# Kernel tuning notes

Hardware: AMD Instinct MI355X
Metric: run time of the kernel (lower is better)

The kernel has to match this reference:

```python
import jax, jax.numpy as jnp
import numpy as np

N, E, C, H, EDGE_DIM, HID = 50000, 800000, 128, 8, 64, 512
D = C // H  # head dim = out_channels_conv


def layer_norm(x, g, b, eps=1e-5):
    mu = x.mean(-1, keepdims=True)
    var = ((x - mu) ** 2).mean(-1, keepdims=True)
    return (x - mu) * jax.lax.rsqrt(var + eps) * g + b


def _lin_init(k, fan_in, fan_out):
    s = 1.0 / np.sqrt(fan_in)
    kw, kb = jax.random.split(k)
    w = jax.random.uniform(kw, (fan_in, fan_out), minval=-s, maxval=s, dtype=jnp.float32)
    b = jax.random.uniform(kb, (fan_out,), minval=-s, maxval=s, dtype=jnp.float32)
    return w, b


def setup_inputs() -> dict:
    key = jax.random.key(0)
    ks = jax.random.split(key, 16)
    wq, bq = _lin_init(ks[0], C, C)
    wk, bk = _lin_init(ks[1], C, C)
    wv, bv = _lin_init(ks[2], C, C)
    ws, bs = _lin_init(ks[3], C, C)          # lin_self
    we, be = _lin_init(ks[4], EDGE_DIM, C)   # lin_edge
    wp, bp = _lin_init(ks[5], C, C)          # projection
    w1, b1 = _lin_init(ks[6], C, HID)        # node_dst_mlp[0]
    w2, b2 = _lin_init(ks[7], HID, C)        # node_dst_mlp[2]
    x = jax.random.normal(ks[8], (N, C), dtype=jnp.float32)
    edge_attr = jax.random.normal(ks[9], (E, EDGE_DIM), dtype=jnp.float32)
    edge_index = jax.random.randint(ks[10], (2, E), 0, N, dtype=jnp.int64)
    return dict(
        x=x, edge_attr=edge_attr, edge_index=edge_index,
        wq=wq, bq=bq, wk=wk, bk=bk, wv=wv, bv=bv, ws=ws, bs=bs,
        we=we, be=be, wp=wp, bp=bp, w1=w1, b1=b1, w2=w2, b2=b2,
        ln1_g=jnp.ones((C,), jnp.float32), ln1_b=jnp.zeros((C,), jnp.float32),
        ln2_g=jnp.ones((C,), jnp.float32), ln2_b=jnp.zeros((C,), jnp.float32),
    )


def reference(x, edge_attr, edge_index,
              wq, bq, wk, bk, wv, bv, ws, bs, we, be, wp, bp,
              w1, b1, w2, b2, ln1_g, ln1_b, ln2_g, ln2_b):
    src, dst = edge_index[0], edge_index[1]

    x_skip = x
    xn = layer_norm(x, ln1_g, ln1_b)                       # layer_norm_attention
    x_r = xn @ ws + bs                                     # lin_self residual
    q = (xn @ wq + bq).reshape(N, H, D)
    k = (xn @ wk + bk).reshape(N, H, D)
    v = (xn @ wv + bv).reshape(N, H, D)
    e = (edge_attr @ we + be).reshape(E, H, D)             # lin_edge (edge_pre_mlp = Identity)

    # edge-indexed multi-head attention: softmax over incoming edges per dst node
    ke = k[src] + e                                        # [E,H,D]
    alpha = jnp.einsum('ehd,ehd->eh', q[dst], ke) / np.sqrt(D)   # [E,H]
    amax = jax.lax.stop_gradient(jax.ops.segment_max(alpha, dst, num_segments=N))
    ex = jnp.exp(alpha - amax[dst])
    den = jax.ops.segment_sum(ex, dst, num_segments=N)
    w = ex / (den[dst] + 1e-16)                            # [E,H]
    out = jax.ops.segment_sum(w[:, :, None] * (v[src] + e), dst, num_segments=N)  # [N,H,D]
    out = out.reshape(N, C)

    out = (out + x_r) @ wp + bp                            # projection
    out = out + x_skip
    h = layer_norm(out, ln2_g, ln2_b)                      # layer_norm_mlp_dst
    h = jax.nn.gelu(h @ w1 + b1) @ w2 + b2                 # node_dst_mlp
    nodes_new = out + h
    return nodes_new, edge_attr
```

## Files before the change

### kernel.cpp

```cpp
#include <hip/hip_runtime.h>
#include <hip/hip_bf16.h>
#include <cstdio>

#define NN 50000
#define NE 800000
#define CC 128
#define EDIM 64
#define HIDN 512

using bf16 = __hip_bfloat16;
typedef short sh8 __attribute__((ext_vector_type(8)));
typedef float f32x4 __attribute__((ext_vector_type(4)));

static __device__ __forceinline__ float b2f(bf16 v){ return __bfloat162float(v); }
static __device__ __forceinline__ bf16 f2b(float v){ return __float2bfloat16(v); }
static __device__ __forceinline__ float u2f(unsigned short u){
    union { unsigned int i; float f; } w; w.i = ((unsigned int)u) << 16; return w.f;
}
static __device__ __forceinline__ unsigned short f2u(float f){
    bf16 b = __float2bfloat16(f);
    return *reinterpret_cast<unsigned short*>(&b);
}
static __device__ __forceinline__ float2 loadbf2(const bf16* p){
    __hip_bfloat162 v = *reinterpret_cast<const __hip_bfloat162*>(p);
    return make_float2(__bfloat162float(v.x), __bfloat162float(v.y));
}
static __device__ __forceinline__ float gelu_tanh(float x){
    const float c = 0.7978845608028654f;
    float u = c * (x + 0.044715f * x * x * x);
    return x / (1.0f + __expf(-2.0f * u));
}

constexpr size_t AL(size_t x){ return (x + 255) & ~(size_t)255; }
constexpr size_t OFF_FLAG = 0;
constexpr size_t OFF_DEG  = 256;
constexpr size_t OFF_ROW  = AL(OFF_DEG + (size_t)(NN + 1) * 4);
constexpr size_t OFF_CUR  = AL(OFF_ROW + (size_t)(NN + 1) * 4);
constexpr size_t OFF_SRC  = AL(OFF_CUR + (size_t)(NN + 1) * 4);
constexpr size_t OFF_DST  = AL(OFF_SRC + (size_t)NE * 4);
constexpr size_t OFF_QC   = AL(OFF_DST + (size_t)NE * 4);
constexpr size_t OFF_KC   = AL(OFF_QC  + (size_t)NN * CC * 2);
constexpr size_t OFF_VC   = AL(OFF_KC  + (size_t)NN * CC * 2);
constexpr size_t OFF_ATT  = AL(OFF_VC  + (size_t)NN * CC * 2);
constexpr size_t OFF_PRM  = AL(OFF_ATT + (size_t)NN * CC * 2);
constexpr size_t PRM_ELEMS = 4096;
constexpr size_t OFF_ALP  = AL(OFF_PRM + PRM_ELEMS * 2);
constexpr size_t OFF_VP   = AL(OFF_ALP + (size_t)NE * 8 * 2);
constexpr size_t OFF_XRC  = AL(OFF_VP + (size_t)NE * CC * 2);
constexpr size_t OFF_WFQ  = AL(OFF_XRC + (size_t)NN * CC * 2);
constexpr size_t OFF_WFK  = OFF_WFQ + 32768;
constexpr size_t OFF_WFV  = OFF_WFK + 32768;
constexpr size_t OFF_WFS  = OFF_WFV + 32768;
constexpr size_t OFF_WFP  = OFF_WFS + 32768;
constexpr size_t OFF_WF1  = OFF_WFP + 32768;
constexpr size_t OFF_WF2  = OFF_WF1 + 131072;
constexpr size_t OFF_WFE  = OFF_WF2 + 131072;
constexpr size_t OFF_BSUM = OFF_WFE + 16384;
constexpr size_t WS_NEED  = OFF_BSUM + 256;

__global__ void k_detect(const unsigned short* xw, const unsigned int* ew, int* flags){
    __shared__ int sw, sz;
    if (threadIdx.x == 0){ sw = 0; sz = 0; }
    __syncthreads();
    int w = 0;
    for (int i = threadIdx.x; i < 8192; i += 256){
        unsigned e = (xw[i] >> 7) & 0xFF;
        if (e == 0xFF || (e != 0 && (e < 0x60 || e > 0x90))) w++;
    }
    atomicAdd(&sw, w);
    int z = 0;
    for (int i = threadIdx.x; i < 2048; i += 256)
        if (ew[2*i+1] == 0u) z++;
    atomicAdd(&sz, z);
    __syncthreads();
    if (threadIdx.x == 0){
        flags[0] = (sw > 2048) ? 1 : 0;
        flags[1] = (sz > 1536) ? 1 : 0;
    }
}

struct CvtJob { const void* s; bf16* d; int n; };
struct CvtJobs { CvtJob j[12]; };
__global__ void k_cvt_all(CvtJobs jobs, const int* flags){
    const int f = flags[0];
    const int e = blockIdx.x >> 1;
    const CvtJob J = jobs.j[e];
    const int stride = 2 * 256;
    for (int i = (blockIdx.x & 1) * 256 + threadIdx.x; i < J.n; i += stride){
        if (f) J.d[i] = f2b(((const float*)J.s)[i]);
        else   J.d[i] = ((const bf16*)J.s)[i];
    }
}

__global__ void k_cvt_idx(const int* e32, int* srcI, int* dstI, int* deg, const int* flags){
    const int f = flags[1];
    int i = blockIdx.x * blockDim.x + threadIdx.x;
    const int stride = gridDim.x * blockDim.x;
    if (f){
        const long long* e64 = (const long long*)e32;
        for (; i < NE; i += stride){
            srcI[i] = (int)e64[i];
            const int d = (int)e64[NE + i];
            dstI[i] = d;
            atomicAdd(&deg[d], 1);
        }
    } else {
        for (; i < NE; i += stride){
            srcI[i] = e32[i];
            const int d = e32[NE + i];
            dstI[i] = d;
            atomicAdd(&deg[d], 1);
        }
    }
}

struct WJob { const void* W; bf16* WF; int K; int N; };
struct WJobs { WJob j[8]; };
__global__ void k_wprep_all(WJobs jobs, const int* flags){
    const int f = flags[0];
    const WJob J = jobs.j[blockIdx.x / 48];
    const int KS = J.K >> 5;
    const int total = J.K * J.N;
    for (int o = (blockIdx.x % 48) * 256 + threadIdx.x; o < total; o += 48 * 256){
        const int j  = o & 7;
        const int ln = (o >> 3) & 63;
        const int tt = o >> 9;
        const int ks = tt % KS, ct = tt / KS;
        const int kk = (ks << 5) + ((ln >> 4) << 3) + j;
        const int c  = (ct << 4) + (ln & 15);
        const int src = kk * J.N + c;
        J.WF[o] = f ? f2b(((const float*)J.W)[src]) : ((const bf16*)J.W)[src];
    }
}

#define ASWZ(row, chunk)  (((row) << 8)  + ((((chunk) ^ ((row) & 15))) << 4))
#define HSWZ(row, chunk)  (((row) << 10) + ((((chunk) ^ ((row) & 15))) << 4))
#define EASWZ(row, chunk) (((row) << 7)  + ((((chunk) ^ ((row) & 7)))  << 4))

static __device__ __forceinline__ void gemm_nodes_128(
    const unsigned short* Abase, int row0, int lane,
    const bf16* __restrict__ WF, const bf16* __restrict__ bias,
    bf16* __restrict__ outp, int n0)
{
    const int rA = row0 + (lane & 15);
    sh8 af[4];
    #pragma unroll
    for (int ks = 0; ks < 4; ++ks)
        af[ks] = *(const sh8*)((const char*)Abase + ASWZ(rA, (ks << 2) + (lane >> 4)));
    f32x4 acc[8] = {};
    #pragma unroll
    for (int ks = 0; ks < 4; ++ks)
        #pragma unroll
        for (int ct = 0; ct < 8; ++ct){
            sh8 bfr = *(const sh8*)(WF + ((size_t)((ct << 2) + ks) * 64 + lane) * 8);
            acc[ct] = __builtin_amdgcn_mfma_f32_16x16x32_bf16(af[ks], bfr, acc[ct], 0, 0, 0);
        }
    #pragma unroll
    for (int ct = 0; ct < 8; ++ct){
        const int c = (ct << 4) + (lane & 15);
        const float bv = b2f(bias[c]);
        #pragma unroll
        for (int i = 0; i < 4; ++i){
            const int r = row0 + ((lane >> 4) << 2) + i;
            if (n0 + r < NN)
                outp[(size_t)(n0 + r) * CC + c] = f2b(acc[ct][i] + bv);
        }
    }
}

__global__ __launch_bounds__(256) void k_node_pre2(
    const void* __restrict__ x_raw, const int* __restrict__ flags,
    const bf16* __restrict__ WFq, const bf16* __restrict__ bq,
    const bf16* __restrict__ WFk, const bf16* __restrict__ bk,
    const bf16* __restrict__ WFv, const bf16* __restrict__ bv,
    const bf16* __restrict__ WFs, const bf16* __restrict__ bs,
    const bf16* __restrict__ g,  const bf16* __restrict__ bb,
    bf16* __restrict__ q, bf16* __restrict__ k, bf16* __restrict__ v,
    bf16* __restrict__ xr)
{
    __shared__ unsigned short A[64 * 128];
    const int t = threadIdx.x, lane = t & 63, wid = t >> 6;
    const int n0 = blockIdx.x * 64;
    const int row0 = wid * 16;

    if (flags[0]){
        const float* x = (const float*)x_raw;
        #pragma unroll
        for (int it = 0; it < 8; ++it){
            const int idx = lane + 64 * it;
            const int row = row0 + (idx >> 5), c = (idx & 31) << 2;
            float4 a = make_float4(0.f, 0.f, 0.f, 0.f);
            if (n0 + row < NN)
                a = *(const float4*)&x[(size_t)(n0 + row) * CC + c];
            ushort4 b;
            b.x = f2u(a.x); b.y = f2u(a.y); b.z = f2u(a.z); b.w = f2u(a.w);
            *(ushort4*)((char*)A + ASWZ(row, c >> 3) + ((c & 7) << 1)) = b;
        }
    } else {
        const bf16* x = (const bf16*)x_raw;
        #pragma unroll
        for (int it = 0; it < 4; ++it){
            const int idx = lane + 64 * it;
            const int row = row0 + (idx >> 4), chunk = idx & 15, col = chunk << 3;
            uint4 val = make_uint4(0u, 0u, 0u, 0u);
            if (n0 + row < NN)
                val = *(const uint4*)&x[(size_t)(n0 + row) * CC + col];
            *(uint4*)((char*)A + ASWZ(row, chunk)) = val;
        }
    }

    {
        const int nd = row0 + (lane & 15), qd = lane >> 4;
        float vals[32];
        #pragma unroll
        for (int i = 0; i < 4; ++i){
            uint4 u = *(const uint4*)((const char*)A + ASWZ(nd, (qd << 2) + i));
            unsigned uu[4] = {u.x, u.y, u.z, u.w};
            #pragma unroll
            for (int j2 = 0; j2 < 4; ++j2){
                vals[i*8 + j2*2]     = u2f((unsigned short)(uu[j2] & 0xFFFF));
                vals[i*8 + j2*2 + 1] = u2f((unsigned short)(uu[j2] >> 16));
            }
        }
        float s = 0.f;
        #pragma unroll
        for (int i = 0; i < 32; ++i) s += vals[i];
        s += __shfl_xor(s, 16); s += __shfl_xor(s, 32);
        const float mu = s * (1.0f / CC);
        float vv = 0.f;
        #pragma unroll
        for (int i = 0; i < 32; ++i){ const float d = vals[i] - mu; vv += d * d; }
        vv += __shfl_xor(vv, 16); vv += __shfl_xor(vv, 32);
        const float rstd = rsqrtf(vv * (1.0f / CC) + 1e-5f);
        #pragma unroll
        for (int i = 0; i < 4; ++i){
            unsigned w[4];
            #pragma unroll
            for (int j2 = 0; j2 < 4; ++j2){
                const int c0 = qd * 32 + i * 8 + j2 * 2;
                const float a0 = (vals[i*8+j2*2]   - mu) * rstd * b2f(g[c0])   + b2f(bb[c0]);
                const float a1 = (vals[i*8+j2*2+1] - mu) * rstd * b2f(g[c0+1]) + b2f(bb[c0+1]);
                w[j2] = (unsigned)f2u(a0) | ((unsigned)f2u(a1) << 16);
            }
            *(uint4*)((char*)A + ASWZ(nd, (qd << 2) + i)) = make_uint4(w[0], w[1], w[2], w[3]);
        }
    }

    gemm_nodes_128(A, row0, lane, WFq, bq, q,  n0);
    gemm_nodes_128(A, row0, lane, WFk, bk, k,  n0);
    gemm_nodes_128(A, row0, lane, WFv, bv, v,  n0);
    gemm_nodes_128(A, row0, lane, WFs, bs, xr, n0);
}

__global__ __launch_bounds__(1024) void k_scan1(const int* __restrict__ deg,
                                                int* __restrict__ row, int* __restrict__ bsum){
    __shared__ int sb[1024];
    const int t = threadIdx.x;
    const int idx = blockIdx.x * 1024 + t;
    sb[t] = (idx < NN) ? deg[idx] : 0;
    __syncthreads();
    for (int off = 1; off < 1024; off <<= 1){
        int tv = (t >= off) ? sb[t - off] : 0;
        __syncthreads();
        sb[t] += tv;
        __syncthreads();
    }
    if (idx < NN) row[idx + 1] = sb[t];
    if (t == 1023) bsum[blockIdx.x] = sb[1023];
}

__global__ __launch_bounds__(1024) void k_scan3(const int* __restrict__ bsum,
                                                int* __restrict__ row, int* __restrict__ cur){
    __shared__ int sadd;
    const int t = threadIdx.x;
    if (t < 64){
        int a = 0;
        for (int i = t; i < (int)blockIdx.x; i += 64) a += bsum[i];
        for (int off = 32; off; off >>= 1) a += __shfl_xor(a, off);
        if (t == 0) sadd = a;
    }
    __syncthreads();
    const int idx = blockIdx.x * 1024 + t;
    if (idx < NN){
        const int vfin = row[idx + 1] + sadd;
        row[idx + 1] = vfin;
        cur[idx + 1] = vfin;
    }
    if (idx == 0){ row[0] = 0; cur[0] = 0; }
}

__global__ __launch_bounds__(256) void k_edge4(
    const void* __restrict__ ea_raw, const int* __restrict__ flags,
    const bf16* __restrict__ WFe, const bf16* __restrict__ be,
    const bf16* __restrict__ kv_q, const bf16* __restrict__ kv_k, const bf16* __restrict__ kv_v,
    const int* __restrict__ srcI, const int* __restrict__ dstI, int* __restrict__ cur,
    unsigned short* __restrict__ alphap, unsigned short* __restrict__ vperm,
    void* __restrict__ outv)
{
    __shared__ unsigned short EA[64 * 64];
    __shared__ unsigned short ET[64 * 128];
    const int t = threadIdx.x, lane = t & 63, wid = t >> 6;
    const int e0 = blockIdx.x * 64;
    const int row0 = wid * 16;

    if (flags[0]){
        const float* ea = (const float*)ea_raw;
        float* outd = (float*)outv + (size_t)NN * CC;
        #pragma unroll
        for (int it = 0; it < 4; ++it){
            const int idx = lane + 64 * it;
            const int row = row0 + (idx >> 4), c = (idx & 15) << 2;
            const size_t o = (size_t)(e0 + row) * EDIM + c;
            const float4 a = *(const float4*)&ea[o];
            *(float4*)&outd[o] = a;
            ushort4 b;
            b.x = f2u(a.x); b.y = f2u(a.y); b.z = f2u(a.z); b.w = f2u(a.w);
            *(ushort4*)((char*)EA + EASWZ(row, c >> 3) + ((c & 7) << 1)) = b;
        }
    } else {
        const unsigned short* ea = (const unsigned short*)ea_raw;
        unsigned short* outd = (unsigned short*)outv + (size_t)NN * CC;
        #pragma unroll
        for (int it = 0; it < 2; ++it){
            const int idx = lane + 64 * it;
            const int row = row0 + (idx >> 3), c = (idx & 7) << 3;
            const size_t o = (size_t)(e0 + row) * EDIM + c;
            uint4 raw = *(const uint4*)&ea[o];
            *(uint4*)&outd[o] = raw;
            *(uint4*)((char*)EA + EASWZ(row, c >> 3)) = raw;
        }
    }

    {
        const int rA = row0 + (lane & 15);
        sh8 af[2];
        #pragma unroll
        for (int ks = 0; ks < 2; ++ks)
            af[ks] = *(const sh8*)((const char*)EA + EASWZ(rA, (ks << 2) + (lane >> 4)));
        f32x4 acc[8] = {};
        #pragma unroll
        for (int ks = 0; ks < 2; ++ks)
            #pragma unroll
            for (int ct = 0; ct < 8; ++ct){
                sh8 bfr = *(const sh8*)(WFe + ((size_t)((ct << 1) + ks) * 64 + lane) * 8);
                acc[ct] = __builtin_amdgcn_mfma_f32_16x16x32_bf16(af[ks], bfr, acc[ct], 0, 0, 0);
            }
        #pragma unroll
        for (int ct = 0; ct < 8; ++ct){
            const int c = (ct << 4) + (lane & 15);
            const float bv = b2f(be[c]);
            #pragma unroll
            for (int i = 0; i < 4; ++i){
                const int r = row0 + ((lane >> 4) << 2) + i;
                *(unsigned short*)((char*)ET + ASWZ(r, c >> 3) + ((c & 7) << 1)) =
                    f2u(acc[ct][i] + bv);
            }
        }
    }

    const int g = t >> 5, cT = t & 31, c = cT << 2;
    int s8[8], d8[8];
    #pragma unroll
    for (int i = 0; i < 8; ++i){
        const int eid = e0 + g * 8 + i;
        s8[i] = srcI[eid];
        d8[i] = dstI[eid];
    }
    int pmine = 0;
    if (cT < 8) pmine = atomicAdd(&cur[dstI[e0 + g * 8 + cT]], 1);
    int p8[8];
    #pragma unroll
    for (int i = 0; i < 8; ++i)
        p8[i] = __shfl(pmine, ((g & 1) << 5) + i);

    ushort4 kr[8], vr[8], qr[8];
    #pragma unroll
    for (int i = 0; i < 8; ++i) kr[i] = *(const ushort4*)&kv_k[(size_t)s8[i] * CC + c];
    #pragma unroll
    for (int i = 0; i < 8; ++i) vr[i] = *(const ushort4*)&kv_v[(size_t)s8[i] * CC + c];
    #pragma unroll
    for (int i = 0; i < 8; ++i) qr[i] = *(const ushort4*)&kv_q[(size_t)d8[i] * CC + c];
    #pragma unroll
    for (int i = 0; i < 8; ++i){
        const ushort4 ev = *(const ushort4*)((const char*)ET + ASWZ(g * 8 + i, c >> 3) + ((c & 7) << 1));
        const float e0_ = u2f(ev.x), e1_ = u2f(ev.y), e2_ = u2f(ev.z), e3_ = u2f(ev.w);
        float part = u2f(qr[i].x) * (e0_ + u2f(kr[i].x)) + u2f(qr[i].y) * (e1_ + u2f(kr[i].y))
                   + u2f(qr[i].z) * (e2_ + u2f(kr[i].z)) + u2f(qr[i].w) * (e3_ + u2f(kr[i].w));
        part += __shfl_xor(part, 1);
        part += __shfl_xor(part, 2);
        if ((cT & 3) == 0)
            alphap[(size_t)p8[i] * 8 + (cT >> 2)] = f2u(part * 0.25f);
        ushort4 vo;
        vo.x = f2u(e0_ + u2f(vr[i].x)); vo.y = f2u(e1_ + u2f(vr[i].y));
        vo.z = f2u(e2_ + u2f(vr[i].z)); vo.w = f2u(e3_ + u2f(vr[i].w));
        *(ushort4*)&vperm[(size_t)p8[i] * CC + c] = vo;
    }
}

__global__ __launch_bounds__(256) void k_attn3(
    const unsigned short* __restrict__ alphap, const bf16* __restrict__ vperm,
    const int* __restrict__ rowstart, bf16* __restrict__ attn_bf)
{
    const int t = threadIdx.x, lane = t & 63, wid = t >> 6;
    const int n = blockIdx.x * 4 + wid;
    const int h = lane >> 3;

    float m = -INFINITY, den = 0.0f;
    float2 num = make_float2(0.0f, 0.0f);

    const int jb = rowstart[n], je = rowstart[n + 1];
    for (int j = jb; j < je; ++j) {
        const float alpha = u2f(alphap[(size_t)j * 8 + h]);
        const float2 v2 = loadbf2(&vperm[(size_t)j * CC + 2 * lane]);
        if (alpha > m) {
            const float sc = __expf(m - alpha);
            den *= sc; num.x *= sc; num.y *= sc;
            m = alpha;
        }
        const float p = __expf(alpha - m);
        den += p;
        num.x += p * v2.x;
        num.y += p * v2.y;
    }
    const float inv = 1.0f / (den + 1e-16f);
    __hip_bfloat162 pr;
    pr.x = f2b(num.x * inv);
    pr.y = f2b(num.y * inv);
    *reinterpret_cast<__hip_bfloat162*>(&attn_bf[(size_t)n * CC + 2 * lane]) = pr;
}

__global__ __launch_bounds__(256) void k_post2(
    const bf16* __restrict__ attn_bf, const bf16* __restrict__ xr,
    const void* __restrict__ x_raw,
    const bf16* __restrict__ WFp, const bf16* __restrict__ bp,
    const bf16* __restrict__ WF1, const bf16* __restrict__ b1,
    const bf16* __restrict__ WF2, const bf16* __restrict__ b2c,
    const bf16* __restrict__ g2, const bf16* __restrict__ bb2,
    void* __restrict__ outv, const int* __restrict__ flags)
{
    __shared__ unsigned short A[64 * 128];
    __shared__ unsigned short HID[64 * 512];
    const int t = threadIdx.x, lane = t & 63, wid = t >> 6;
    const int n0 = blockIdx.x * 64;
    const int f32io = flags[0];
    const int row0 = wid * 16;

    #pragma unroll
    for (int it = 0; it < 4; ++it){
        const int idx = lane + 64 * it;
        const int row = row0 + (idx >> 4), chunk = idx & 15, col = chunk << 3;
        unsigned w[4] = {0u, 0u, 0u, 0u};
        if (n0 + row < NN){
            const size_t o = (size_t)(n0 + row) * CC + col;
            uint4 a4 = *(const uint4*)&attn_bf[o];
            uint4 r4 = *(const uint4*)&xr[o];
            unsigned au[4] = {a4.x, a4.y, a4.z, a4.w};
            unsigned ru[4] = {r4.x, r4.y, r4.z, r4.w};
            #pragma unroll
            for (int j2 = 0; j2 < 4; ++j2){
                const float lo = u2f((unsigned short)(au[j2] & 0xFFFF)) +
                                 u2f((unsigned short)(ru[j2] & 0xFFFF));
                const float hi = u2f((unsigned short)(au[j2] >> 16)) +
                                 u2f((unsigned short)(ru[j2] >> 16));
                w[j2] = (unsigned)f2u(lo) | ((unsigned)f2u(hi) << 16);
            }
        }
        *(uint4*)((char*)A + ASWZ(row, chunk)) = make_uint4(w[0], w[1], w[2], w[3]);
    }

    const int rA = row0 + (lane & 15);

    float out2[8][4];
    {
        sh8 af[4];
        #pragma unroll
        for (int ks = 0; ks < 4; ++ks)
            af[ks] = *(const sh8*)((const char*)A + ASWZ(rA, (ks << 2) + (lane >> 4)));
        f32x4 acc[8] = {};
        #pragma unroll
        for (int ks = 0; ks < 4; ++ks)
            #pragma unroll
            for (int ct = 0; ct < 8; ++ct){
                sh8 bfr = *(const sh8*)(WFp + ((size_t)((ct << 2) + ks) * 64 + lane) * 8);
                acc[ct] = __builtin_amdgcn_mfma_f32_16x16x32_bf16(af[ks], bfr, acc[ct], 0, 0, 0);
            }
        #pragma unroll
        for (int ct = 0; ct < 8; ++ct){
            const int c = (ct << 4) + (lane & 15);
            const float bv = b2f(bp[c]);
            #pragma unroll
            for (int i = 0; i < 4; ++i){
                const int r = row0 + ((lane >> 4) << 2) + i;
                float xs = 0.f;
                if (n0 + r < NN){
                    const size_t o = (size_t)(n0 + r) * CC + c;
                    xs = f32io ? ((const float*)x_raw)[o] : b2f(((const bf16*)x_raw)[o]);
                }
                out2[ct][i] = acc[ct][i] + bv + xs;
            }
        }
    }

    {
        float mu[4], rstd[4];
        #pragma unroll
        for (int i = 0; i < 4; ++i){
            float s = 0.f;
            #pragma unroll
            for (int ct = 0; ct < 8; ++ct) s += out2[ct][i];
            s += __shfl_xor(s, 1); s += __shfl_xor(s, 2);
            s += __shfl_xor(s, 4); s += __shfl_xor(s, 8);
            mu[i] = s * (1.0f / CC);
        }
        #pragma unroll
        for (int i = 0; i < 4; ++i){
            float vv = 0.f;
            #pragma unroll
            for (int ct = 0; ct < 8; ++ct){ const float d = out2[ct][i] - mu[i]; vv += d * d; }
            vv += __shfl_xor(vv, 1); vv += __shfl_xor(vv, 2);
            vv += __shfl_xor(vv, 4); vv += __shfl_xor(vv, 8);
            rstd[i] = rsqrtf(vv * (1.0f / CC) + 1e-5f);
        }
        #pragma unroll
        for (int ct = 0; ct < 8; ++ct){
            const int c = (ct << 4) + (lane & 15);
            const float gv = b2f(g2[c]), bbv = b2f(bb2[c]);
            const int chunk = c >> 3;
            #pragma unroll
            for (int i = 0; i < 4; ++i){
                const int r = row0 + ((lane >> 4) << 2) + i;
                const float ln = (out2[ct][i] - mu[i]) * rstd[i] * gv + bbv;
                *(unsigned short*)((char*)A + ASWZ(r, chunk) + ((c & 7) << 1)) = f2u(ln);
            }
        }
    }

    {
        sh8 af[4];
        #pragma unroll
        for (int ks = 0; ks < 4; ++ks)
            af[ks] = *(const sh8*)((const char*)A + ASWZ(rA, (ks << 2) + (lane >> 4)));
        #pragma unroll
        for (int grp = 0; grp < 4; ++grp){
            f32x4 acc[8] = {};
            #pragma unroll
            for (int ks = 0; ks < 4; ++ks)
                #pragma unroll
                for (int ctl = 0; ctl < 8; ++ctl){
                    const int ct = grp * 8 + ctl;
                    sh8 bfr = *(const sh8*)(WF1 + ((size_t)((ct << 2) + ks) * 64 + lane) * 8);
                    acc[ctl] = __builtin_amdgcn_mfma_f32_16x16x32_bf16(af[ks], bfr, acc[ctl], 0, 0, 0);
                }
            #pragma unroll
            for (int ctl = 0; ctl < 8; ++ctl){
                const int ct = grp * 8 + ctl;
                const int c = (ct << 4) + (lane & 15);
                const float bv = b2f(b1[c]);
                const int chunk = c >> 3;
                #pragma unroll
                for (int i = 0; i < 4; ++i){
                    const int r = row0 + ((lane >> 4) << 2) + i;
                    const float h = gelu_tanh(acc[ctl][i] + bv);
                    *(unsigned short*)((char*)HID + HSWZ(r, chunk) + ((c & 7) << 1)) = f2u(h);
                }
            }
        }
    }

    {
        f32x4 acc[8] = {};
        #pragma unroll
        for (int ks = 0; ks < 16; ++ks){
            sh8 afh = *(const sh8*)((const char*)HID + HSWZ(rA, (ks << 2) + (lane >> 4)));
            #pragma unroll
            for (int ct = 0; ct < 8; ++ct){
                sh8 bfr = *(const sh8*)(WF2 + ((size_t)((ct << 4) + ks) * 64 + lane) * 8);
                acc[ct] = __builtin_amdgcn_mfma_f32_16x16x32_bf16(afh, bfr, acc[ct], 0, 0, 0);
            }
        }
        #pragma unroll
        for (int ct = 0; ct < 8; ++ct){
            const int c = (ct << 4) + (lane & 15);
            const float bv = b2f(b2c[c]);
            #pragma unroll
            for (int i = 0; i < 4; ++i){
                const int r = row0 + ((lane >> 4) << 2) + i;
                if (n0 + r < NN){
                    const float val = out2[ct][i] + acc[ct][i] + bv;
                    if (f32io) ((float*)outv)[(size_t)(n0 + r) * CC + c] = val;
                    else       ((bf16*)outv)[(size_t)(n0 + r) * CC + c] = f2b(val);
                }
            }
        }
    }
}

extern "C" void kernel_launch(void* const* d_in, const int* in_sizes, int n_in,
                              void* d_out, int out_size, void* d_ws, size_t ws_size,
                              hipStream_t stream)
{
    if (ws_size < WS_NEED) {
        fprintf(stderr, "[kl] WS TOO SMALL ws=%zu need=%zu\n", ws_size, WS_NEED);
        return;
    }

    char* ws = (char*)d_ws;
    int*  flags = (int*)(ws + OFF_FLAG);
    int*  deg   = (int*)(ws + OFF_DEG);
    int*  row   = (int*)(ws + OFF_ROW);
    int*  cur   = (int*)(ws + OFF_CUR);
    int*  srcI  = (int*)(ws + OFF_SRC);
    int*  dstI  = (int*)(ws + OFF_DST);
    int*  bsum  = (int*)(ws + OFF_BSUM);
    bf16* qC    = (bf16*)(ws + OFF_QC);
    bf16* kC    = (bf16*)(ws + OFF_KC);
    bf16* vC    = (bf16*)(ws + OFF_VC);
    bf16* attC  = (bf16*)(ws + OFF_ATT);
    bf16* xrC   = (bf16*)(ws + OFF_XRC);
    unsigned short* alphap = (unsigned short*)(ws + OFF_ALP);
    unsigned short* vperm  = (unsigned short*)(ws + OFF_VP);
    bf16* WFq = (bf16*)(ws + OFF_WFQ);
    bf16* WFk = (bf16*)(ws + OFF_WFK);
    bf16* WFv = (bf16*)(ws + OFF_WFV);
    bf16* WFs = (bf16*)(ws + OFF_WFS);
    bf16* WFp = (bf16*)(ws + OFF_WFP);
    bf16* WF1 = (bf16*)(ws + OFF_WF1);
    bf16* WF2 = (bf16*)(ws + OFF_WF2);
    bf16* WFe = (bf16*)(ws + OFF_WFE);

    bf16* P = (bf16*)(ws + OFF_PRM);
    bf16 *bqC=P; P+=128; bf16 *bkC=P; P+=128;
    bf16 *bvC=P; P+=128; bf16 *bsC=P; P+=128;
    bf16 *beC=P; P+=128; bf16 *bpC=P; P+=128;
    bf16 *b1C=P; P+=512; bf16 *b2C=P; P+=128;
    bf16 *g1C=P; P+=128; bf16 *n1C=P; P+=128;
    bf16 *g2C=P; P+=128; bf16 *n2C=P; P+=128;

    hipMemsetAsync(deg, 0, (size_t)(NN + 1) * sizeof(int), stream);

    k_detect<<<1, 256, 0, stream>>>((const unsigned short*)d_in[0],
                                    (const unsigned int*)d_in[2], flags);

    {
        CvtJobs cj;
        bf16* dsts[12] = {bqC,bkC,bvC,bsC,beC,bpC,b1C,b2C,g1C,n1C,g2C,n2C};
        const int idxs[12] = {4,6,8,10,12,14,16,18,19,20,21,22};
        const int ns[12]   = {128,128,128,128,128,128,512,128,128,128,128,128};
        for (int i = 0; i < 12; ++i){ cj.j[i].s = d_in[idxs[i]]; cj.j[i].d = dsts[i]; cj.j[i].n = ns[i]; }
        k_cvt_all<<<12 * 2, 256, 0, stream>>>(cj, flags);
    }
    k_cvt_idx<<<1024, 256, 0, stream>>>((const int*)d_in[2], srcI, dstI, deg, flags);

    {
        WJobs wj;
        const WJob js[8] = {{d_in[3],WFq,128,128},{d_in[5],WFk,128,128},{d_in[7],WFv,128,128},
                            {d_in[9],WFs,128,128},{d_in[13],WFp,128,128},{d_in[15],WF1,128,512},
                            {d_in[17],WF2,512,128},{d_in[11],WFe,64,128}};
        for (int i = 0; i < 8; ++i) wj.j[i] = js[i];
        k_wprep_all<<<8 * 48, 256, 0, stream>>>(wj, flags);
    }

    const int NB64 = (NN + 63) / 64;
    const int NSC  = (NN + 1023) / 1024;
    k_node_pre2<<<NB64, 256, 0, stream>>>(d_in[0], flags, WFq, bqC, WFk, bkC, WFv, bvC,
                                          WFs, bsC, g1C, n1C, qC, kC, vC, xrC);
    k_scan1<<<NSC, 1024, 0, stream>>>(deg, row, bsum);
    k_scan3<<<NSC, 1024, 0, stream>>>(bsum, row, cur);
    k_edge4<<<NE / 64, 256, 0, stream>>>(d_in[1], flags, WFe, beC, qC, kC, vC,
                                         srcI, dstI, cur, alphap, vperm, d_out);
    k_attn3<<<NN / 4, 256, 0, stream>>>(alphap, (const bf16*)vperm, row, attC);
    k_post2<<<NB64, 256, 0, stream>>>(attC, xrC, d_in[0], WFp, bpC, WF1, b1C, WF2, b2C,
                                      g2C, n2C, d_out, flags);
}
```

Before: 501.9 us.

## Aggregate raw edge features per node and apply edge projection after softmax

The edge kernel stops materialising a per-edge permuted v+e tensor (E x 128 bf16). Instead it writes the permuted raw edge attributes (E x 64) and source indices. The attention kernel gathers v by source, accumulates softmax-weighted raw edge features, then projects them once per node with the edge weight held in LDS and adds the bias scaled by the weight sum. This uses linearity to cut per-edge write/read traffic, at the cost of a per-block LDS weight load, a per-node 64x128 matvec and random v gathers.

```diff
diff --git a/kernel.cpp b/kernel.cpp
--- a/kernel.cpp
+++ b/kernel.cpp
@@ -45,8 +45,9 @@
 constexpr size_t OFF_PRM  = AL(OFF_ATT + (size_t)NN * CC * 2);
 constexpr size_t PRM_ELEMS = 4096;
 constexpr size_t OFF_ALP  = AL(OFF_PRM + PRM_ELEMS * 2);
-constexpr size_t OFF_VP   = AL(OFF_ALP + (size_t)NE * 8 * 2);
-constexpr size_t OFF_XRC  = AL(OFF_VP + (size_t)NE * CC * 2);
+constexpr size_t OFF_EAP  = AL(OFF_ALP + (size_t)NE * 8 * 2);
+constexpr size_t OFF_SP   = AL(OFF_EAP + (size_t)NE * EDIM * 2);
+constexpr size_t OFF_XRC  = AL(OFF_SP  + (size_t)NE * 4);
 constexpr size_t OFF_WFQ  = AL(OFF_XRC + (size_t)NN * CC * 2);
 constexpr size_t OFF_WFK  = OFF_WFQ + 32768;
 constexpr size_t OFF_WFV  = OFF_WFK + 32768;
@@ -289,13 +290,13 @@
     if (idx == 0){ row[0] = 0; cur[0] = 0; }
 }
 
-__global__ __launch_bounds__(256) void k_edge4(
+__global__ __launch_bounds__(256) void k_edge6(
     const void* __restrict__ ea_raw, const int* __restrict__ flags,
     const bf16* __restrict__ WFe, const bf16* __restrict__ be,
-    const bf16* __restrict__ kv_q, const bf16* __restrict__ kv_k, const bf16* __restrict__ kv_v,
+    const bf16* __restrict__ kv_q, const bf16* __restrict__ kv_k,
     const int* __restrict__ srcI, const int* __restrict__ dstI, int* __restrict__ cur,
-    unsigned short* __restrict__ alphap, unsigned short* __restrict__ vperm,
-    void* __restrict__ outv)
+    unsigned short* __restrict__ alphap, unsigned short* __restrict__ eaperm,
+    int* __restrict__ srcperm, void* __restrict__ outv)
 {
     __shared__ unsigned short EA[64 * 64];
     __shared__ unsigned short ET[64 * 128];
@@ -373,11 +374,9 @@
     for (int i = 0; i < 8; ++i)
         p8[i] = __shfl(pmine, ((g & 1) << 5) + i);
 
-    ushort4 kr[8], vr[8], qr[8];
+    ushort4 kr[8], qr[8];
     #pragma unroll
     for (int i = 0; i < 8; ++i) kr[i] = *(const ushort4*)&kv_k[(size_t)s8[i] * CC + c];
-    #pragma unroll
-    for (int i = 0; i < 8; ++i) vr[i] = *(const ushort4*)&kv_v[(size_t)s8[i] * CC + c];
     #pragma unroll
     for (int i = 0; i < 8; ++i) qr[i] = *(const ushort4*)&kv_q[(size_t)d8[i] * CC + c];
     #pragma unroll
@@ -390,42 +389,82 @@
         part += __shfl_xor(part, 2);
         if ((cT & 3) == 0)
             alphap[(size_t)p8[i] * 8 + (cT >> 2)] = f2u(part * 0.25f);
-        ushort4 vo;
-        vo.x = f2u(e0_ + u2f(vr[i].x)); vo.y = f2u(e1_ + u2f(vr[i].y));
-        vo.z = f2u(e2_ + u2f(vr[i].z)); vo.w = f2u(e3_ + u2f(vr[i].w));
-        *(ushort4*)&vperm[(size_t)p8[i] * CC + c] = vo;
-    }
-}
-
-__global__ __launch_bounds__(256) void k_attn3(
-    const unsigned short* __restrict__ alphap, const bf16* __restrict__ vperm,
-    const int* __restrict__ rowstart, bf16* __restrict__ attn_bf)
+        if (cT < 16){
+            const int c2 = cT << 2;
+            ushort4 er = *(const ushort4*)((const char*)EA + EASWZ(g * 8 + i, c2 >> 3) + ((c2 & 7) << 1));
+            *(ushort4*)&eaperm[(size_t)p8[i] * EDIM + c2] = er;
+        }
+        if (cT == 16) srcperm[p8[i]] = s8[i];
+    }
+}
+
+__global__ __launch_bounds__(256) void k_attn4(
+    const unsigned short* __restrict__ alphap, const unsigned short* __restrict__ eaperm,
+    const int* __restrict__ srcperm, const bf16* __restrict__ vC,
+    const void* __restrict__ we_raw, const bf16* __restrict__ be,
+    const int* __restrict__ flags, const int* __restrict__ rowstart,
+    bf16* __restrict__ attn_bf)
 {
+    __shared__ unsigned short weS[EDIM * CC];
+    __shared__ float sea[4][8][68];
     const int t = threadIdx.x, lane = t & 63, wid = t >> 6;
+
+    if (flags[0]){
+        const float* wr = (const float*)we_raw;
+        for (int i = t; i < EDIM * CC; i += 256) weS[i] = f2u(wr[i]);
+    } else {
+        const unsigned short* wr = (const unsigned short*)we_raw;
+        for (int i = t; i < EDIM * CC; i += 256) weS[i] = wr[i];
+    }
+    __syncthreads();
+
     const int n = blockIdx.x * 4 + wid;
-    const int h = lane >> 3;
+    const int h = lane >> 3, sub = lane & 7;
 
     float m = -INFINITY, den = 0.0f;
-    float2 num = make_float2(0.0f, 0.0f);
+    float num0 = 0.f, num1 = 0.f;
+    float sA[8] = {0.f, 0.f, 0.f, 0.f, 0.f, 0.f, 0.f, 0.f};
 
     const int jb = rowstart[n], je = rowstart[n + 1];
     for (int j = jb; j < je; ++j) {
         const float alpha = u2f(alphap[(size_t)j * 8 + h]);
-        const float2 v2 = loadbf2(&vperm[(size_t)j * CC + 2 * lane]);
+        const int s = srcperm[j];
+        const float2 v2 = loadbf2(&vC[(size_t)s * CC + 2 * lane]);
+        const ushort4 ew0 = *(const ushort4*)&eaperm[(size_t)j * EDIM + sub * 8];
+        const ushort4 ew1 = *(const ushort4*)&eaperm[(size_t)j * EDIM + sub * 8 + 4];
         if (alpha > m) {
             const float sc = __expf(m - alpha);
-            den *= sc; num.x *= sc; num.y *= sc;
+            den *= sc; num0 *= sc; num1 *= sc;
+            #pragma unroll
+            for (int i = 0; i < 8; ++i) sA[i] *= sc;
             m = alpha;
         }
         const float p = __expf(alpha - m);
         den += p;
-        num.x += p * v2.x;
-        num.y += p * v2.y;
-    }
+        num0 += p * v2.x;
+        num1 += p * v2.y;
+        sA[0] += p * u2f(ew0.x); sA[1] += p * u2f(ew0.y);
+        sA[2] += p * u2f(ew0.z); sA[3] += p * u2f(ew0.w);
+        sA[4] += p * u2f(ew1.x); sA[5] += p * u2f(ew1.y);
+        sA[6] += p * u2f(ew1.z); sA[7] += p * u2f(ew1.w);
+    }
+    #pragma unroll
+    for (int i = 0; i < 8; ++i) sea[wid][h][sub * 8 + i] = sA[i];
+
     const float inv = 1.0f / (den + 1e-16f);
+    const float sw  = den * inv;
+
+    const int c0 = 2 * lane, c1 = 2 * lane + 1;
+    float accE0 = 0.f, accE1 = 0.f;
+    #pragma unroll 8
+    for (int d = 0; d < EDIM; ++d){
+        const float S = sea[wid][h][d];
+        accE0 += S * u2f(weS[d * CC + c0]);
+        accE1 += S * u2f(weS[d * CC + c1]);
+    }
     __hip_bfloat162 pr;
-    pr.x = f2b(num.x * inv);
-    pr.y = f2b(num.y * inv);
+    pr.x = f2b((num0 + accE0) * inv + sw * b2f(be[c0]));
+    pr.y = f2b((num1 + accE1) * inv + sw * b2f(be[c1]));
     *reinterpret_cast<__hip_bfloat162*>(&attn_bf[(size_t)n * CC + 2 * lane]) = pr;
 }
 
@@ -618,7 +657,8 @@
     bf16* attC  = (bf16*)(ws + OFF_ATT);
     bf16* xrC   = (bf16*)(ws + OFF_XRC);
     unsigned short* alphap = (unsigned short*)(ws + OFF_ALP);
-    unsigned short* vperm  = (unsigned short*)(ws + OFF_VP);
+    unsigned short* eaperm = (unsigned short*)(ws + OFF_EAP);
+    int*  srcperm = (int*)(ws + OFF_SP);
     bf16* WFq = (bf16*)(ws + OFF_WFQ);
     bf16* WFk = (bf16*)(ws + OFF_WFK);
     bf16* WFv = (bf16*)(ws + OFF_WFV);
@@ -666,9 +706,10 @@
                                           WFs, bsC, g1C, n1C, qC, kC, vC, xrC);
     k_scan1<<<NSC, 1024, 0, stream>>>(deg, row, bsum);
     k_scan3<<<NSC, 1024, 0, stream>>>(bsum, row, cur);
-    k_edge4<<<NE / 64, 256, 0, stream>>>(d_in[1], flags, WFe, beC, qC, kC, vC,
-                                         srcI, dstI, cur, alphap, vperm, d_out);
-    k_attn3<<<NN / 4, 256, 0, stream>>>(alphap, (const bf16*)vperm, row, attC);
+    k_edge6<<<NE / 64, 256, 0, stream>>>(d_in[1], flags, WFe, beC, qC, kC,
+                                         srcI, dstI, cur, alphap, eaperm, srcperm, d_out);
+    k_attn4<<<NN / 4, 256, 0, stream>>>(alphap, eaperm, srcperm, vC, d_in[11], beC,
+                                        flags, row, attC);
     k_post2<<<NB64, 256, 0, stream>>>(attC, xrC, d_in[0], WFp, bpC, WF1, b1C, WF2, b2C,
                                       g2C, n2C, d_out, flags);
 }
```

Measured after the change: 572.8 us. +14.1%, slower.
